# Optimization experiments

Hardware: AMD Instinct MI355X
Metric: run time of the kernel (lower is better)

Reference implementation:

```python
import jax, jax.numpy as jnp
import numpy as np

NOTE_RES = 64  # global constant in the original repo; equals D of rep


def _down(x):
    # conv1d with kernel [0.5, 0.5], stride 2 over last axis (even length)
    return 0.5 * (x[..., ::2] + x[..., 1::2])


def setup_inputs() -> dict:
    key = jax.random.key(0)
    k1, k2, k3 = jax.random.split(key, 3)
    B, D, T = 32, NOTE_RES, 4096
    rep = jax.random.normal(k1, (B, D, T), dtype=jnp.float32)
    duration_mask = jax.random.uniform(k2, (B, D, T), dtype=jnp.float32)
    position_mask = jax.random.uniform(k3, (B, D, T), dtype=jnp.float32)
    return {
        "rep": rep,
        "duration_mask": duration_mask,
        "position_mask": position_mask,
        "low_duration": 1,
        "up_duration": 64,
    }


def reference(rep, duration_mask, position_mask, low_duration, up_duration):
    B, D, T = rep.shape  # D == NOTE_RES
    x = jnp.transpose(rep, (0, 2, 1))  # [B, T, NOTE_RES]; conv axis is last
    densed = _down(x)                  # [B, T, NOTE_RES//2]
    pot = NOTE_RES // 2
    res = jnp.zeros((B, T), dtype=rep.dtype)
    for i in range(0, NOTE_RES - low_duration):
        win_len = NOTE_RES - i - 1
        if win_len == pot:
            # descend one pyramid level
            x = densed
            densed = _down(x) if i < NOTE_RES - 2 else None
            d = x  # [B, T, win_len]
            pot //= 2
        else:
            pad_len = win_len - pot
            # mix fine-resolution prefix with coarse suffix -> length win_len
            d = jnp.concatenate([x[..., : 2 * pad_len], densed[..., pad_len:]], axis=-1)
        if win_len < up_duration:
            # sum_w d[b,t,w] * position_mask[b,w,t], gated by duration_mask[b,win_len-1,t]
            contrib = duration_mask[:, win_len - 1, :] * jnp.einsum(
                "btw,bwt->bt", d, position_mask[:, :win_len, :]
            )
            res = res + contrib
    return res[:, None, :]  # [B, 1, T]
```

## Files before the change

kernel.cpp:

```cpp
#include <hip/hip_runtime.h>


#define TT 4096

__device__ __forceinline__ void async_load_f32(const float* g, float* l) {
  __builtin_amdgcn_global_load_lds(
      (const __attribute__((address_space(1))) void*)g,
      (__attribute__((address_space(3))) void*)l, 4, 0, 0);
}

template <int P0, int P1>
__device__ __forceinline__ float role32(const float* __restrict__ lrep,
                                        const float* __restrict__ lpm,
                                        const float* dmr, int lane, int low,
                                        int up) {
  float xa[32 - P0];
#pragma unroll
  for (int k = P0; k < 32; ++k)
    xa[k - P0] = 0.5f * (lrep[(2 * k) * 64 + lane] + lrep[(2 * k + 1) * 64 + lane]);
  float q[P1 - 1];
#pragma unroll
  for (int j = 0; j < P1 - 1; ++j)
    q[j] = lrep[(2 * j) * 64 + lane] * lpm[(2 * j) * 64 + lane] +
           lrep[(2 * j + 1) * 64 + lane] * lpm[(2 * j + 1) * 64 + lane];
  float p = 0.f;
#pragma unroll
  for (int j = 0; j < P0; ++j) p += q[j];
  float res = 0.f;
#pragma unroll
  for (int pad = P0; pad < P1; ++pad) {
    const int L = 32 + pad;
    float s = p;
#pragma unroll
    for (int k = pad; k < 32; ++k)
      s = fmaf(xa[k - P0], lpm[(k + pad) * 64 + lane], s);
    if (L >= low && L < up) res = fmaf(dmr[pad - P0], s, res);
    if (pad + 1 < P1) p += q[pad];
  }
  return res;
}

template <int M>
__device__ __forceinline__ void down_lds(const float* __restrict__ lpm, int lane,
                                         float* xa, float* q) {
#pragma unroll
  for (int j = 0; j < M; ++j) {
    const float a = xa[2 * j];
    const float c = xa[2 * j + 1];
    q[j] = a * lpm[(2 * j) * 64 + lane] + c * lpm[(2 * j + 1) * 64 + lane];
    xa[j] = 0.5f * (a + c);
  }
}

template <int M>
__device__ __forceinline__ void acc_lds(const float* __restrict__ lpm,
                                        const float* dmr, int lane,
                                        const float* xa, const float* q, int low,
                                        int up, float& res) {
  float p = 0.f;
#pragma unroll
  for (int pad = 0; pad < M; ++pad) {
    const int L = M + pad;
    float s = p;
#pragma unroll
    for (int k = pad; k < M; ++k) s = fmaf(xa[k], lpm[(k + pad) * 64 + lane], s);
    if (L >= low && L < up) res = fmaf(dmr[M - 1 + pad], s, res);
    p += q[pad];
  }
}

__device__ __forceinline__ float role_tail(const float* __restrict__ lrep,
                                           const float* __restrict__ lpm,
                                           const float* dmr, int lane, int low,
                                           int up) {
  float xa[32];
#pragma unroll
  for (int k = 0; k < 32; ++k)
    xa[k] = 0.5f * (lrep[(2 * k) * 64 + lane] + lrep[(2 * k + 1) * 64 + lane]);
  float q[16];
  float res = 0.f;
  down_lds<16>(lpm, lane, xa, q);
  acc_lds<16>(lpm, dmr, lane, xa, q, low, up, res);
  down_lds<8>(lpm, lane, xa, q);
  acc_lds<8>(lpm, dmr, lane, xa, q, low, up, res);
  down_lds<4>(lpm, lane, xa, q);
  acc_lds<4>(lpm, dmr, lane, xa, q, low, up, res);
  down_lds<2>(lpm, lane, xa, q);
  acc_lds<2>(lpm, dmr, lane, xa, q, low, up, res);
  down_lds<1>(lpm, lane, xa, q);
  acc_lds<1>(lpm, dmr, lane, xa, q, low, up, res);
  return res;
}

__global__ __launch_bounds__(256, 4) void ContextGenerator_34875134444049_kernel(
    const float* __restrict__ rep, const float* __restrict__ dm,
    const float* __restrict__ pm, const int* __restrict__ lowp,
    const int* __restrict__ upp, float* __restrict__ out) {
  __shared__ float lds[128 * 64 + 4 * 64];
  const int wid = threadIdx.x >> 6;
  const int lane = threadIdx.x & 63;
  const int b = blockIdx.x >> 6;
  const int t0 = (blockIdx.x & 63) << 6;

  const size_t base = (size_t)b * 64 * TT + (size_t)t0;

  for (int r = wid; r < 127; r += 4) {
    const float* src = (r < 64) ? rep + base + (size_t)r * TT
                                : pm + base + (size_t)(r - 64) * TT;
    async_load_f32(src + lane, &lds[r * 64]);
  }

  const int low = lowp[0];
  const int up = upp[0];

  const float* dmb = dm + base + lane;
  float dmr[31];
  if (wid == 0) {
#pragma unroll
    for (int i = 0; i < 6; ++i) dmr[i] = dmb[(size_t)(31 + i) * TT];
  } else if (wid == 1) {
#pragma unroll
    for (int i = 0; i < 7; ++i) dmr[i] = dmb[(size_t)(37 + i) * TT];
  } else if (wid == 2) {
#pragma unroll
    for (int i = 0; i < 19; ++i) dmr[i] = dmb[(size_t)(44 + i) * TT];
  } else {
#pragma unroll
    for (int i = 0; i < 31; ++i) dmr[i] = dmb[(size_t)i * TT];
  }

  __syncthreads();

  const float* lrep = lds;
  const float* lpm = lds + 64 * 64;

  float res;
  if (wid == 0)
    res = role32<0, 6>(lrep, lpm, dmr, lane, low, up);
  else if (wid == 1)
    res = role32<6, 13>(lrep, lpm, dmr, lane, low, up);
  else if (wid == 2)
    res = role32<13, 32>(lrep, lpm, dmr, lane, low, up);
  else
    res = role_tail(lrep, lpm, dmr, lane, low, up);

  float* part = lds + 128 * 64;
  part[wid * 64 + lane] = res;
  __syncthreads();

  if (threadIdx.x < 64) {
    const float r = part[threadIdx.x] + part[64 + threadIdx.x] +
                    part[128 + threadIdx.x] + part[192 + threadIdx.x];
    out[(size_t)b * TT + t0 + threadIdx.x] = r;
  }
}

extern "C" void kernel_launch(void* const* d_in, const int* in_sizes, int n_in,
                              void* d_out, int out_size, void* d_ws,
                              size_t ws_size, hipStream_t stream) {
  const float* rep = (const float*)d_in[0];
  const float* dm = (const float*)d_in[1];
  const float* pm = (const float*)d_in[2];
  const int* lowp = (const int*)d_in[3];
  const int* upp = (const int*)d_in[4];
  float* out = (float*)d_out;

  const int blocks = out_size / 64;
  ContextGenerator_34875134444049_kernel<<<blocks, 256, 0, stream>>>(
      rep, dm, pm, lowp, upp, out);
}
```

Baseline: 125.9 us.

## Double-buffer LDS staging so each block processes four time tiles with prefetch

Each block now handles four consecutive 64-wide time tiles instead of one. It uses two LDS buffers so the async global-to-LDS load of the next tile overlaps compute on the current one. The row-62 position-mask value is loaded into a register so each buffer holds 126 rows, and the final reduction folds into wave 3. In exchange the grid is a quarter the size, LDS use doubles, and occupancy drops (launch bounds 2). That can reduce latency hiding on a memory-bound kernel.

```diff
diff --git a/kernel.cpp b/kernel.cpp
--- a/kernel.cpp
+++ b/kernel.cpp
@@ -2,6 +2,8 @@
 
 
 #define TT 4096
+#define ROWS 126
+#define BUFF (ROWS * 64)
 
 __device__ __forceinline__ void async_load_f32(const float* g, float* l) {
   __builtin_amdgcn_global_load_lds(
@@ -9,11 +11,40 @@
       (__attribute__((address_space(3))) void*)l, 4, 0, 0);
 }
 
+__device__ __forceinline__ void stage(const float* __restrict__ rep,
+                                      const float* __restrict__ pm, size_t base,
+                                      float* buf, int wid, int lane) {
+  for (int r = wid; r < ROWS; r += 4) {
+    const float* src = (r < 64) ? rep + base + (size_t)r * TT
+                                : pm + base + (size_t)(r - 64) * TT;
+    async_load_f32(src + lane, &buf[r * 64]);
+  }
+}
+
+__device__ __forceinline__ void load_dm(const float* __restrict__ dmb,
+                                        const float* __restrict__ pmb, int wid,
+                                        float* dmr, float& pm62) {
+  if (wid == 0) {
+#pragma unroll
+    for (int i = 0; i < 6; ++i) dmr[i] = dmb[(size_t)(31 + i) * TT];
+  } else if (wid == 1) {
+#pragma unroll
+    for (int i = 0; i < 7; ++i) dmr[i] = dmb[(size_t)(37 + i) * TT];
+  } else if (wid == 2) {
+#pragma unroll
+    for (int i = 0; i < 19; ++i) dmr[i] = dmb[(size_t)(44 + i) * TT];
+    pm62 = pmb[(size_t)62 * TT];
+  } else {
+#pragma unroll
+    for (int i = 0; i < 31; ++i) dmr[i] = dmb[(size_t)i * TT];
+  }
+}
+
 template <int P0, int P1>
 __device__ __forceinline__ float role32(const float* __restrict__ lrep,
                                         const float* __restrict__ lpm,
-                                        const float* dmr, int lane, int low,
-                                        int up) {
+                                        const float* dmr, float pm62, int lane,
+                                        int low, int up) {
   float xa[32 - P0];
 #pragma unroll
   for (int k = P0; k < 32; ++k)
@@ -32,8 +63,10 @@
     const int L = 32 + pad;
     float s = p;
 #pragma unroll
-    for (int k = pad; k < 32; ++k)
-      s = fmaf(xa[k - P0], lpm[(k + pad) * 64 + lane], s);
+    for (int k = pad; k < 32; ++k) {
+      const float pv = (k + pad == 62) ? pm62 : lpm[(k + pad) * 64 + lane];
+      s = fmaf(xa[k - P0], pv, s);
+    }
     if (L >= low && L < up) res = fmaf(dmr[pad - P0], s, res);
     if (pad + 1 < P1) p += q[pad];
   }
@@ -92,66 +125,69 @@
   return res;
 }
 
-__global__ __launch_bounds__(256, 4) void ContextGenerator_34875134444049_kernel(
+__device__ __forceinline__ float compute_role(const float* __restrict__ buf,
+                                              const float* dmr, float pm62,
+                                              int wid, int lane, int low,
+                                              int up) {
+  const float* lrep = buf;
+  const float* lpm = buf + 64 * 64;
+  if (wid == 0) return role32<0, 6>(lrep, lpm, dmr, 0.f, lane, low, up);
+  if (wid == 1) return role32<6, 13>(lrep, lpm, dmr, 0.f, lane, low, up);
+  if (wid == 2) return role32<13, 32>(lrep, lpm, dmr, pm62, lane, low, up);
+  return role_tail(lrep, lpm, dmr, lane, low, up);
+}
+
+__global__ __launch_bounds__(256, 2) void ContextGenerator_34875134444049_kernel(
     const float* __restrict__ rep, const float* __restrict__ dm,
     const float* __restrict__ pm, const int* __restrict__ lowp,
     const int* __restrict__ upp, float* __restrict__ out) {
-  __shared__ float lds[128 * 64 + 4 * 64];
+  __shared__ float lds[2 * BUFF + 192];
   const int wid = threadIdx.x >> 6;
   const int lane = threadIdx.x & 63;
-  const int b = blockIdx.x >> 6;
-  const int t0 = (blockIdx.x & 63) << 6;
-
-  const size_t base = (size_t)b * 64 * TT + (size_t)t0;
-
-  for (int r = wid; r < 127; r += 4) {
-    const float* src = (r < 64) ? rep + base + (size_t)r * TT
-                                : pm + base + (size_t)(r - 64) * TT;
-    async_load_f32(src + lane, &lds[r * 64]);
-  }
+  const int b = blockIdx.x >> 4;
+  const int c0 = (blockIdx.x & 15) << 2;
+  const size_t bbase = (size_t)b * 64 * TT;
+  float* part = lds + 2 * BUFF;
 
   const int low = lowp[0];
   const int up = upp[0];
 
-  const float* dmb = dm + base + lane;
-  float dmr[31];
-  if (wid == 0) {
-#pragma unroll
-    for (int i = 0; i < 6; ++i) dmr[i] = dmb[(size_t)(31 + i) * TT];
-  } else if (wid == 1) {
-#pragma unroll
-    for (int i = 0; i < 7; ++i) dmr[i] = dmb[(size_t)(37 + i) * TT];
-  } else if (wid == 2) {
-#pragma unroll
-    for (int i = 0; i < 19; ++i) dmr[i] = dmb[(size_t)(44 + i) * TT];
-  } else {
-#pragma unroll
-    for (int i = 0; i < 31; ++i) dmr[i] = dmb[(size_t)i * TT];
-  }
-
-  __syncthreads();
-
-  const float* lrep = lds;
-  const float* lpm = lds + 64 * 64;
-
-  float res;
-  if (wid == 0)
-    res = role32<0, 6>(lrep, lpm, dmr, lane, low, up);
-  else if (wid == 1)
-    res = role32<6, 13>(lrep, lpm, dmr, lane, low, up);
-  else if (wid == 2)
-    res = role32<13, 32>(lrep, lpm, dmr, lane, low, up);
-  else
-    res = role_tail(lrep, lpm, dmr, lane, low, up);
-
-  float* part = lds + 128 * 64;
-  part[wid * 64 + lane] = res;
-  __syncthreads();
-
-  if (threadIdx.x < 64) {
-    const float r = part[threadIdx.x] + part[64 + threadIdx.x] +
-                    part[128 + threadIdx.x] + part[192 + threadIdx.x];
-    out[(size_t)b * TT + t0 + threadIdx.x] = r;
+  float dmrA[31], dmrB[31];
+  float pm62A = 0.f, pm62B = 0.f;
+
+  {
+    const size_t base0 = bbase + ((size_t)(c0 + 0) << 6);
+    stage(rep, pm, base0, lds, wid, lane);
+    load_dm(dm + base0 + lane, pm + base0 + lane, wid, dmrA, pm62A);
+  }
+
+  for (int p = 0; p < 2; ++p) {
+    const int s0 = 2 * p;
+    __syncthreads();
+    {
+      const size_t basen = bbase + ((size_t)(c0 + s0 + 1) << 6);
+      stage(rep, pm, basen, lds + BUFF, wid, lane);
+      load_dm(dm + basen + lane, pm + basen + lane, wid, dmrB, pm62B);
+    }
+    const float r0 = compute_role(lds, dmrA, pm62A, wid, lane, low, up);
+    if (wid < 3) part[wid * 64 + lane] = r0;
+    __syncthreads();
+    if (wid == 3)
+      out[(size_t)b * TT + ((size_t)(c0 + s0) << 6) + lane] =
+          r0 + part[lane] + part[64 + lane] + part[128 + lane];
+
+    __syncthreads();
+    if (p == 0) {
+      const size_t basen = bbase + ((size_t)(c0 + s0 + 2) << 6);
+      stage(rep, pm, basen, lds, wid, lane);
+      load_dm(dm + basen + lane, pm + basen + lane, wid, dmrA, pm62A);
+    }
+    const float r1 = compute_role(lds + BUFF, dmrB, pm62B, wid, lane, low, up);
+    if (wid < 3) part[wid * 64 + lane] = r1;
+    __syncthreads();
+    if (wid == 3)
+      out[(size_t)b * TT + ((size_t)(c0 + s0 + 1) << 6) + lane] =
+          r1 + part[lane] + part[64 + lane] + part[128 + lane];
   }
 }
 
@@ -165,7 +201,7 @@
   const int* upp = (const int*)d_in[4];
   float* out = (float*)d_out;
 
-  const int blocks = out_size / 64;
+  const int blocks = out_size / 256;
   ContextGenerator_34875134444049_kernel<<<blocks, 256, 0, stream>>>(
       rep, dm, pm, lowp, upp, out);
 }
```

Result: slower. 142.5 us (+13.2%).

## Stage duration mask through LDS with 16-byte async global-to-LDS loads

Applied to the files above, without the earlier changes.

Loads rep, position_mask and the duration_mask rows into LDS using 16-byte-per-lane global_load_lds, four rows per wave instruction, instead of 4-byte loads plus per-wave register loads of the duration mask. Each wave then reads its duration-mask values from LDS. The final reduction lets wave 3 add its own result in registers rather than writing it to LDS first. LDS use grows to about 49KB per block and launch bounds drop to 3 blocks per CU, which can reduce occupancy. The whole duration-mask tile, including rows no wave uses, is now fetched.

```diff
diff --git a/kernel.cpp b/kernel.cpp
--- a/kernel.cpp
+++ b/kernel.cpp
@@ -3,17 +3,17 @@
 
 #define TT 4096
 
-__device__ __forceinline__ void async_load_f32(const float* g, float* l) {
+__device__ __forceinline__ void async_load16(const float* g, float* l) {
   __builtin_amdgcn_global_load_lds(
       (const __attribute__((address_space(1))) void*)g,
-      (__attribute__((address_space(3))) void*)l, 4, 0, 0);
+      (__attribute__((address_space(3))) void*)l, 16, 0, 0);
 }
 
 template <int P0, int P1>
 __device__ __forceinline__ float role32(const float* __restrict__ lrep,
                                         const float* __restrict__ lpm,
-                                        const float* dmr, int lane, int low,
-                                        int up) {
+                                        const float* __restrict__ ldm, int lane,
+                                        int low, int up) {
   float xa[32 - P0];
 #pragma unroll
   for (int k = P0; k < 32; ++k)
@@ -34,7 +34,8 @@
 #pragma unroll
     for (int k = pad; k < 32; ++k)
       s = fmaf(xa[k - P0], lpm[(k + pad) * 64 + lane], s);
-    if (L >= low && L < up) res = fmaf(dmr[pad - P0], s, res);
+    if (L >= low && L < up)
+      res = fmaf(ldm[(31 + pad) * 64 + lane], s, res);
     if (pad + 1 < P1) p += q[pad];
   }
   return res;
@@ -54,7 +55,7 @@
 
 template <int M>
 __device__ __forceinline__ void acc_lds(const float* __restrict__ lpm,
-                                        const float* dmr, int lane,
+                                        const float* __restrict__ ldm, int lane,
                                         const float* xa, const float* q, int low,
                                         int up, float& res) {
   float p = 0.f;
@@ -64,15 +65,16 @@
     float s = p;
 #pragma unroll
     for (int k = pad; k < M; ++k) s = fmaf(xa[k], lpm[(k + pad) * 64 + lane], s);
-    if (L >= low && L < up) res = fmaf(dmr[M - 1 + pad], s, res);
+    if (L >= low && L < up)
+      res = fmaf(ldm[(M - 1 + pad) * 64 + lane], s, res);
     p += q[pad];
   }
 }
 
 __device__ __forceinline__ float role_tail(const float* __restrict__ lrep,
                                            const float* __restrict__ lpm,
-                                           const float* dmr, int lane, int low,
-                                           int up) {
+                                           const float* __restrict__ ldm,
+                                           int lane, int low, int up) {
   float xa[32];
 #pragma unroll
   for (int k = 0; k < 32; ++k)
@@ -80,79 +82,63 @@
   float q[16];
   float res = 0.f;
   down_lds<16>(lpm, lane, xa, q);
-  acc_lds<16>(lpm, dmr, lane, xa, q, low, up, res);
+  acc_lds<16>(lpm, ldm, lane, xa, q, low, up, res);
   down_lds<8>(lpm, lane, xa, q);
-  acc_lds<8>(lpm, dmr, lane, xa, q, low, up, res);
+  acc_lds<8>(lpm, ldm, lane, xa, q, low, up, res);
   down_lds<4>(lpm, lane, xa, q);
-  acc_lds<4>(lpm, dmr, lane, xa, q, low, up, res);
+  acc_lds<4>(lpm, ldm, lane, xa, q, low, up, res);
   down_lds<2>(lpm, lane, xa, q);
-  acc_lds<2>(lpm, dmr, lane, xa, q, low, up, res);
+  acc_lds<2>(lpm, ldm, lane, xa, q, low, up, res);
   down_lds<1>(lpm, lane, xa, q);
-  acc_lds<1>(lpm, dmr, lane, xa, q, low, up, res);
+  acc_lds<1>(lpm, ldm, lane, xa, q, low, up, res);
   return res;
 }
 
-__global__ __launch_bounds__(256, 4) void ContextGenerator_34875134444049_kernel(
+__global__ __launch_bounds__(256, 3) void ContextGenerator_34875134444049_kernel(
     const float* __restrict__ rep, const float* __restrict__ dm,
     const float* __restrict__ pm, const int* __restrict__ lowp,
     const int* __restrict__ upp, float* __restrict__ out) {
-  __shared__ float lds[128 * 64 + 4 * 64];
+  __shared__ float lds[192 * 64 + 192];
   const int wid = threadIdx.x >> 6;
   const int lane = threadIdx.x & 63;
   const int b = blockIdx.x >> 6;
   const int t0 = (blockIdx.x & 63) << 6;
-
   const size_t base = (size_t)b * 64 * TT + (size_t)t0;
 
-  for (int r = wid; r < 127; r += 4) {
-    const float* src = (r < 64) ? rep + base + (size_t)r * TT
-                                : pm + base + (size_t)(r - 64) * TT;
-    async_load_f32(src + lane, &lds[r * 64]);
+  const size_t lv = (size_t)(lane >> 4) * TT + (size_t)((lane & 15) << 2);
+  for (int g = wid; g < 48; g += 4) {
+    const float* tbase = (g < 16) ? rep + base
+                       : (g < 32) ? pm + base - (size_t)64 * TT
+                                  : dm + base - (size_t)128 * TT;
+    const float* src = tbase + (size_t)(g << 2) * TT + lv;
+    async_load16(src, &lds[g * 256]);
   }
 
   const int low = lowp[0];
   const int up = upp[0];
 
-  const float* dmb = dm + base + lane;
-  float dmr[31];
-  if (wid == 0) {
-#pragma unroll
-    for (int i = 0; i < 6; ++i) dmr[i] = dmb[(size_t)(31 + i) * TT];
-  } else if (wid == 1) {
-#pragma unroll
-    for (int i = 0; i < 7; ++i) dmr[i] = dmb[(size_t)(37 + i) * TT];
-  } else if (wid == 2) {
-#pragma unroll
-    for (int i = 0; i < 19; ++i) dmr[i] = dmb[(size_t)(44 + i) * TT];
-  } else {
-#pragma unroll
-    for (int i = 0; i < 31; ++i) dmr[i] = dmb[(size_t)i * TT];
-  }
-
   __syncthreads();
 
   const float* lrep = lds;
   const float* lpm = lds + 64 * 64;
+  const float* ldm = lds + 128 * 64;
+  float* part = lds + 192 * 64;
 
   float res;
   if (wid == 0)
-    res = role32<0, 6>(lrep, lpm, dmr, lane, low, up);
+    res = role32<0, 6>(lrep, lpm, ldm, lane, low, up);
   else if (wid == 1)
-    res = role32<6, 13>(lrep, lpm, dmr, lane, low, up);
+    res = role32<6, 13>(lrep, lpm, ldm, lane, low, up);
   else if (wid == 2)
-    res = role32<13, 32>(lrep, lpm, dmr, lane, low, up);
+    res = role32<13, 32>(lrep, lpm, ldm, lane, low, up);
   else
-    res = role_tail(lrep, lpm, dmr, lane, low, up);
+    res = role_tail(lrep, lpm, ldm, lane, low, up);
 
-  float* part = lds + 128 * 64;
-  part[wid * 64 + lane] = res;
+  if (wid < 3) part[wid * 64 + lane] = res;
   __syncthreads();
-
-  if (threadIdx.x < 64) {
-    const float r = part[threadIdx.x] + part[64 + threadIdx.x] +
-                    part[128 + threadIdx.x] + part[192 + threadIdx.x];
-    out[(size_t)b * TT + t0 + threadIdx.x] = r;
-  }
+  if (wid == 3)
+    out[(size_t)b * TT + t0 + lane] =
+        res + part[lane] + part[64 + lane] + part[128 + lane];
 }
 
 extern "C" void kernel_launch(void* const* d_in, const int* in_sizes, int n_in,
```

New measurement: 123.9 us. About the same (-1.6%).
